# Kernel tuning notes

Measured on AMD Instinct MI355X. Metric: run time of the kernel, lower is better.

Reference implementation:

```python
import jax, jax.numpy as jnp
import numpy as np

EMBED_DIM = 1024
BATCH, SEQ = 4, 2048


def setup_inputs() -> dict:
    key = jax.random.key(0)
    kx, kq, kk, kv = jax.random.split(key, 4)
    return {
        "x": jax.random.normal(kx, (BATCH, SEQ, EMBED_DIM), dtype=jnp.float32),
        "q_weight": jax.random.normal(kq, (EMBED_DIM, EMBED_DIM), dtype=jnp.float32),
        "k_weight": jax.random.normal(kk, (EMBED_DIM, EMBED_DIM), dtype=jnp.float32),
        "v_weight": jax.random.normal(kv, (EMBED_DIM, EMBED_DIM), dtype=jnp.float32),
    }


def reference(x, q_weight, k_weight, v_weight):
    # x: [b, s, d]
    d = x.shape[-1]
    Q = jnp.einsum('bsd,de->bse', x, q_weight)
    K = jnp.einsum('bsd,de->bse', x, k_weight)
    V = jnp.einsum('bsd,de->bse', x, v_weight)
    scores = jnp.einsum('bqe,bke->bqk', Q, K) / jnp.sqrt(jnp.float32(d))
    attn = jax.nn.softmax(scores, axis=-1)
    out = jnp.einsum('bqk,bke->bqe', attn, V)
    return out
```

## Files before the change

### kernel.cpp

```cpp
#include <hip/hip_runtime.h>
#include <hip/hip_bf16.h>


typedef _Float16 half8 __attribute__((ext_vector_type(8)));
typedef _Float16 half4v __attribute__((ext_vector_type(4)));
typedef float f32x16 __attribute__((ext_vector_type(16)));

#define GLOBAL_AS __attribute__((address_space(1)))
#define LDS_AS __attribute__((address_space(3)))

__device__ __forceinline__ void gll16(const _Float16* g, _Float16* l) {
    __builtin_amdgcn_global_load_lds((GLOBAL_AS const void*)g, (LDS_AS void*)l, 16, 0, 0);
}

__device__ __forceinline__ void lgkm0_pin() {
    asm volatile("s_waitcnt lgkmcnt(0)" ::: "memory");
    __builtin_amdgcn_sched_barrier(0);
}

template <int N>
__device__ __forceinline__ void vmwait() {
    if constexpr (N == 0) asm volatile("s_waitcnt vmcnt(0)" ::: "memory");
    else if constexpr (N == 4) asm volatile("s_waitcnt vmcnt(4)" ::: "memory");
    else asm volatile("s_waitcnt vmcnt(8)" ::: "memory");
}

template <int NPROD, int OUTMODE>
__global__ __launch_bounds__(256) void gemm_nt(
    const _Float16* __restrict__ A0, const _Float16* __restrict__ A1,
    const _Float16* __restrict__ B0, const _Float16* __restrict__ B1,
    float* __restrict__ Cf, _Float16* __restrict__ C0, _Float16* __restrict__ C1,
    int lda, int ldb, int ldc, int K,
    long sA, long sB, long sC, float scale, float scale2) {
    constexpr int NTILES = (NPROD == 3) ? 4 : 2;
    constexpr int BUFH = NTILES * 4096;
    __shared__ alignas(16) _Float16 smem[2 * BUFH];

    const int tid = threadIdx.x;
    const int wave = tid >> 6, lane = tid & 63;
    const int wm = (wave >> 1) * 64, wn = (wave & 1) * 64;
    const int q2 = lane >> 5, r32 = lane & 31;

    const long zA = (long)blockIdx.z * sA;
    const long zB = (long)blockIdx.z * sB;
    const long zC = (long)blockIdx.z * sC;

    const float sc = (blockIdx.y * 2 < gridDim.y) ? scale : scale2;

    const int trow = tid >> 2;
    const int tcol = (((tid & 3) - ((tid >> 3) & 3) - ((tid >> 6) & 3)) & 3) * 8;
    const _Float16* gA0 = A0 + zA + (long)(blockIdx.x * 128 + trow) * lda + tcol;
    const _Float16* gB0 = B0 + zB + (long)(blockIdx.y * 128 + trow) * ldb + tcol;
    const _Float16* gA1 = (NPROD == 3) ? (A1 + zA + (long)(blockIdx.x * 128 + trow) * lda + tcol) : nullptr;
    const _Float16* gB1 = (NPROD == 3) ? (B1 + zB + (long)(blockIdx.y * 128 + trow) * ldb + tcol) : nullptr;

    f32x16 acc[2][2];
#pragma unroll
    for (int i = 0; i < 2; ++i)
#pragma unroll
        for (int j = 0; j < 2; ++j)
#pragma unroll
            for (int r = 0; r < 16; ++r) acc[i][j][r] = 0.f;

    const int ldsoff = tid * 8;
    const int fbase = q2 + (r32 >> 1) + (r32 >> 4);

    {
        _Float16* s = smem;
        gll16(gA0, s + ldsoff);
        gll16(gA0 + 64 * lda, s + ldsoff + 2048);
        gll16(gB0, s + 4096 + ldsoff);
        gll16(gB0 + 64 * ldb, s + 4096 + ldsoff + 2048);
        if (NPROD == 3) {
            gll16(gA1, s + 8192 + ldsoff);
            gll16(gA1 + 64 * lda, s + 8192 + ldsoff + 2048);
            gll16(gB1, s + 12288 + ldsoff);
            gll16(gB1 + 64 * ldb, s + 12288 + ldsoff + 2048);
        }
        gA0 += 32; gB0 += 32;
        if (NPROD == 3) { gA1 += 32; gB1 += 32; }
    }

    int buf = 0;
    for (int k0 = 0; k0 < K; k0 += 32) {
        __syncthreads();

        if (k0 + 32 < K) {
            _Float16* s = smem + (buf ^ 1) * BUFH;
            gll16(gA0, s + ldsoff);
            gll16(gA0 + 64 * lda, s + ldsoff + 2048);
            gll16(gB0, s + 4096 + ldsoff);
            gll16(gB0 + 64 * ldb, s + 4096 + ldsoff + 2048);
            if (NPROD == 3) {
                gll16(gA1, s + 8192 + ldsoff);
                gll16(gA1 + 64 * lda, s + 8192 + ldsoff + 2048);
                gll16(gB1, s + 12288 + ldsoff);
                gll16(gB1 + 64 * ldb, s + 12288 + ldsoff + 2048);
            }
            gA0 += 32; gB0 += 32;
            if (NPROD == 3) { gA1 += 32; gB1 += 32; }
        }

        _Float16* sA0 = smem + buf * BUFH;
        _Float16* sB0 = sA0 + 4096;
        _Float16* sA1 = (NPROD == 3) ? sA0 + 8192 : sA0;
        _Float16* sB1 = (NPROD == 3) ? sA0 + 12288 : sA0;
#pragma unroll
        for (int h = 0; h < 2; ++h) {
            half8 a0[2], b0[2], a1[2], b1[2];
#pragma unroll
            for (int i = 0; i < 2; ++i) {
                const int pp = ((fbase + 2 * i + 2 * h) & 3) * 8;
                a0[i] = *(const half8*)(sA0 + (wm + i * 32 + r32) * 32 + pp);
                b0[i] = *(const half8*)(sB0 + (wn + i * 32 + r32) * 32 + pp);
                if (NPROD == 3) {
                    a1[i] = *(const half8*)(sA1 + (wm + i * 32 + r32) * 32 + pp);
                    b1[i] = *(const half8*)(sB1 + (wn + i * 32 + r32) * 32 + pp);
                }
            }
#pragma unroll
            for (int i = 0; i < 2; ++i)
#pragma unroll
                for (int j = 0; j < 2; ++j) {
                    acc[i][j] = __builtin_amdgcn_mfma_f32_32x32x16_f16(a0[i], b0[j], acc[i][j], 0, 0, 0);
                    if (NPROD == 3) {
                        acc[i][j] = __builtin_amdgcn_mfma_f32_32x32x16_f16(a0[i], b1[j], acc[i][j], 0, 0, 0);
                        acc[i][j] = __builtin_amdgcn_mfma_f32_32x32x16_f16(a1[i], b0[j], acc[i][j], 0, 0, 0);
                    }
                }
        }
        buf ^= 1;
    }

    const int crow0 = blockIdx.x * 128 + wm + 4 * q2;
    const int ccol0 = blockIdx.y * 128 + wn + r32;
#pragma unroll
    for (int i = 0; i < 2; ++i)
#pragma unroll
        for (int j = 0; j < 2; ++j)
#pragma unroll
            for (int r = 0; r < 16; ++r) {
                int row = crow0 + i * 32 + (r & 3) + 8 * (r >> 2);
                long off = zC + (long)row * ldc + (ccol0 + j * 32);
                float v = acc[i][j][r] * sc;
                if (OUTMODE == 0) {
                    Cf[off] = v;
                } else if (OUTMODE == 2) {
                    C0[off] = (_Float16)v;
                } else {
                    _Float16 h = (_Float16)v;
                    C0[off] = h;
                    C1[off] = (_Float16)(v - (float)h);
                }
            }
}

__device__ __forceinline__ void ld_a(half8 (&d)[4][2], const _Float16* base,
                                     int wm, int r32, int fbase) {
#pragma unroll
    for (int i = 0; i < 4; ++i)
#pragma unroll
        for (int h = 0; h < 2; ++h)
            d[i][h] = *(const half8*)(base + (wm + 32 * i + r32) * 32 +
                                      ((fbase + 2 * i + 2 * h) & 3) * 8);
}

__device__ __forceinline__ void ld_b(half8 (&d)[2][2], const _Float16* base,
                                     int wn, int r32, int fbase) {
#pragma unroll
    for (int j = 0; j < 2; ++j)
#pragma unroll
        for (int h = 0; h < 2; ++h)
            d[j][h] = *(const half8*)(base + (wn + 32 * j + r32) * 32 +
                                      ((fbase + 2 * j + 2 * h) & 3) * 8);
}

__device__ __forceinline__ void mfma_blk(f32x16 (&acc)[4][2], const half8 (&a)[4][2],
                                         const half8 (&b)[2][2]) {
#pragma unroll
    for (int i = 0; i < 4; ++i)
#pragma unroll
        for (int j = 0; j < 2; ++j) {
            acc[i][j] = __builtin_amdgcn_mfma_f32_32x32x16_f16(a[i][0], b[j][0], acc[i][j], 0, 0, 0);
            acc[i][j] = __builtin_amdgcn_mfma_f32_32x32x16_f16(a[i][1], b[j][1], acc[i][j], 0, 0, 0);
        }
}

__device__ __forceinline__ void stage_tile(_Float16* dst, const _Float16* g, int ld,
                                           int ldsoff) {
    gll16(g, dst + ldsoff);
    gll16(g + (long)128 * ld, dst + 4096 + ldsoff);
}

template <int OUTMODE>
__global__ __launch_bounds__(512, 2) void gemm8p(
    const _Float16* __restrict__ A0, const _Float16* __restrict__ A1,
    const _Float16* __restrict__ B0, const _Float16* __restrict__ B1,
    float* __restrict__ Cf, _Float16* __restrict__ C0, _Float16* __restrict__ C1,
    int lda, int ldb, int ldc, int K,
    long sA, long sB, long sC, float scale, float scale2) {
    __shared__ alignas(16) _Float16 smem[65536];

    const int tid = threadIdx.x;
    const int wave = tid >> 6, lane = tid & 63;
    const int wm = (wave >> 2) * 128, wn = (wave & 3) * 64;
    const int q2 = lane >> 5, r32 = lane & 31;

    const long zA = (long)blockIdx.z * sA;
    const long zB = (long)blockIdx.z * sB;
    const long zC = (long)blockIdx.z * sC;
    const float sc = (blockIdx.y * 2 < gridDim.y) ? scale : scale2;

    const int trow = tid >> 2;
    const int tcol = (((tid & 3) - ((tid >> 3) & 3) - ((tid >> 6) & 3)) & 3) * 8;
    const _Float16* gA0 = A0 + zA + (long)(blockIdx.x * 256 + trow) * lda + tcol;
    const _Float16* gB0 = B0 + zB + (long)(blockIdx.y * 256 + trow) * ldb + tcol;
    const _Float16* gA1 = A1 + zA + (long)(blockIdx.x * 256 + trow) * lda + tcol;
    const _Float16* gB1 = B1 + zB + (long)(blockIdx.y * 256 + trow) * ldb + tcol;

    const int ldsoff = tid * 8;
    const int fbase = q2 + (r32 >> 1) + (r32 >> 4);

    f32x16 acc[4][2];
#pragma unroll
    for (int i = 0; i < 4; ++i)
#pragma unroll
        for (int j = 0; j < 2; ++j)
#pragma unroll
            for (int r = 0; r < 16; ++r) acc[i][j][r] = 0.f;

    const int nT = K >> 5;

    {
        _Float16* s = smem;
        stage_tile(s + 0, gA0, lda, ldsoff);
        stage_tile(s + 8192, gB0, ldb, ldsoff);
        stage_tile(s + 16384, gA1, lda, ldsoff);
        stage_tile(s + 24576, gB1, ldb, ldsoff);
        gA0 += 32; gB0 += 32; gA1 += 32; gB1 += 32;
        vmwait<0>();
        __builtin_amdgcn_s_barrier();
    }

    int buf = 0;
    for (int t = 0; t < nT; ++t) {
        _Float16* scur = smem + buf * 32768;
        _Float16* snx = smem + (buf ^ 1) * 32768;
        const bool pre = (t + 1 < nT);

        half8 a0[4][2], b0[2][2], a1[4][2], b1[2][2];

        ld_a(a0, scur, wm, r32, fbase);
        ld_b(b0, scur + 8192, wn, r32, fbase);
        if (pre) {
            stage_tile(snx + 0, gA0, lda, ldsoff);
            stage_tile(snx + 8192, gB0, ldb, ldsoff);
            stage_tile(snx + 16384, gA1, lda, ldsoff);
            stage_tile(snx + 24576, gB1, ldb, ldsoff);
            gA0 += 32; gB0 += 32; gA1 += 32; gB1 += 32;
        }
        __builtin_amdgcn_s_barrier();
        lgkm0_pin();
        __builtin_amdgcn_s_setprio(1);
        mfma_blk(acc, a0, b0);
        __builtin_amdgcn_s_setprio(0);
        __builtin_amdgcn_s_barrier();

        ld_b(b1, scur + 24576, wn, r32, fbase);
        __builtin_amdgcn_s_barrier();
        lgkm0_pin();
        __builtin_amdgcn_s_setprio(1);
        mfma_blk(acc, a0, b1);
        __builtin_amdgcn_s_setprio(0);
        __builtin_amdgcn_s_barrier();

        ld_a(a1, scur + 16384, wm, r32, fbase);
        __builtin_amdgcn_s_barrier();
        lgkm0_pin();
        __builtin_amdgcn_s_setprio(1);
        mfma_blk(acc, a1, b0);
        __builtin_amdgcn_s_setprio(0);
        if (pre) vmwait<0>();
        __builtin_amdgcn_s_barrier();

        buf ^= 1;
    }

    const int crow0 = blockIdx.x * 256 + wm + 4 * q2;
    const int ccol0 = blockIdx.y * 256 + wn + r32;
#pragma unroll
    for (int i = 0; i < 4; ++i)
#pragma unroll
        for (int j = 0; j < 2; ++j)
#pragma unroll
            for (int r = 0; r < 16; ++r) {
                int row = crow0 + i * 32 + (r & 3) + 8 * (r >> 2);
                long off = zC + (long)row * ldc + (ccol0 + j * 32);
                float v = acc[i][j][r] * sc;
                if (OUTMODE == 0) {
                    Cf[off] = v;
                } else {
                    _Float16 h = (_Float16)v;
                    C0[off] = h;
                    C1[off] = (_Float16)(v - (float)h);
                }
            }
}

__global__ __launch_bounds__(256) void prep_fused(
    const float* __restrict__ x, _Float16* __restrict__ x0, _Float16* __restrict__ x1,
    long n4, int nsplit,
    const float* __restrict__ wq, const float* __restrict__ wk,
    const float* __restrict__ wv,
    _Float16* __restrict__ qk0, _Float16* __restrict__ qk1,
    _Float16* __restrict__ v0, _Float16* __restrict__ v1) {
    __shared__ float t[32][33];
    if ((int)blockIdx.x < nsplit) {
        long i = (long)blockIdx.x * 256 + threadIdx.x;
        if (i >= n4) return;
        float4 v = ((const float4*)x)[i];
        float a[4] = {v.x, v.y, v.z, v.w};
        half4v h, l;
#pragma unroll
        for (int c = 0; c < 4; ++c) {
            h[c] = (_Float16)a[c];
            l[c] = (_Float16)(a[c] - (float)h[c]);
        }
        ((half4v*)x0)[i] = h;
        ((half4v*)x1)[i] = l;
        return;
    }
    const int idx = blockIdx.x - nsplit;
    const int z = idx >> 10;
    const int tile = idx & 1023;
    const float* in = (z == 0) ? wq : (z == 1) ? wk : wv;
    _Float16* o0 = (z == 0) ? qk0 : (z == 1) ? qk0 + 1024 * 1024 : v0;
    _Float16* o1 = (z == 0) ? qk1 : (z == 1) ? qk1 + 1024 * 1024 : v1;

    const int c0 = (tile & 31) * 32, r0 = (tile >> 5) * 32;
    const int tx = threadIdx.x & 31, ty = threadIdx.x >> 5;
#pragma unroll
    for (int i = 0; i < 32; i += 8)
        t[ty + i][tx] = in[(long)(r0 + ty + i) * 1024 + c0 + tx];
    __syncthreads();
#pragma unroll
    for (int i = 0; i < 32; i += 8) {
        float v = t[tx][ty + i];
        _Float16 h = (_Float16)v;
        long o = (long)(c0 + ty + i) * 1024 + r0 + tx;
        o0[o] = h;
        o1[o] = (_Float16)(v - (float)h);
    }
}

__global__ __launch_bounds__(256) void softmax_rows(const float* __restrict__ S,
                                                    _Float16* __restrict__ P) {
    const int n = 2048;
    const long base = (long)blockIdx.x * n;
    const float4* row4 = (const float4*)(S + base);
    const int tid = threadIdx.x;
    const int wave = tid >> 6;

    float4 v0 = row4[tid * 2];
    float4 v1 = row4[tid * 2 + 1];
    float v[8] = {v0.x, v0.y, v0.z, v0.w, v1.x, v1.y, v1.z, v1.w};
    float lm = -3.4e38f;
#pragma unroll
    for (int t = 0; t < 8; ++t) lm = fmaxf(lm, v[t]);
#pragma unroll
    for (int o = 32; o > 0; o >>= 1) lm = fmaxf(lm, __shfl_xor(lm, o));
    __shared__ float redm[4];
    __shared__ float reds[4];
    if ((tid & 63) == 0) redm[wave] = lm;
    __syncthreads();
    lm = fmaxf(fmaxf(redm[0], redm[1]), fmaxf(redm[2], redm[3]));

    float e[8];
    float ls = 0.f;
#pragma unroll
    for (int t = 0; t < 8; ++t) {
        e[t] = __expf(v[t] - lm);
        ls += e[t];
    }
#pragma unroll
    for (int o = 32; o > 0; o >>= 1) ls += __shfl_xor(ls, o);
    if ((tid & 63) == 0) reds[wave] = ls;
    __syncthreads();
    ls = reds[0] + reds[1] + reds[2] + reds[3];
    const float inv = 1.f / ls;
    half8 p;
#pragma unroll
    for (int t = 0; t < 8; ++t) p[t] = (_Float16)(e[t] * inv);
    ((half8*)(P + base))[tid] = p;
}

extern "C" void kernel_launch(void* const* d_in, const int* in_sizes, int n_in,
                              void* d_out, int out_size, void* d_ws, size_t ws_size,
                              hipStream_t stream) {
    (void)in_sizes; (void)n_in; (void)out_size; (void)ws_size;
    const float* x = (const float*)d_in[0];
    const float* wq = (const float*)d_in[1];
    const float* wk = (const float*)d_in[2];
    const float* wv = (const float*)d_in[3];
    float* out = (float*)d_out;
    char* ws = (char*)d_ws;

    const long MB = 1l << 20;
    _Float16* Wqk0 = (_Float16*)(ws + 0 * MB);
    _Float16* Wqk1 = (_Float16*)(ws + 4 * MB);
    _Float16* Wv0  = (_Float16*)(ws + 8 * MB);
    _Float16* Wv1  = (_Float16*)(ws + 10 * MB);
    _Float16* x0   = (_Float16*)(ws + 12 * MB);
    _Float16* x1   = (_Float16*)(ws + 28 * MB);
    _Float16* P    = (_Float16*)(ws + 12 * MB);
    _Float16* QK0  = (_Float16*)(ws + 44 * MB);
    _Float16* QK1  = (_Float16*)(ws + 76 * MB);
    _Float16* Vt   = (_Float16*)(ws + 108 * MB);
    float*    S    = (float*)(ws + 124 * MB);

    const int B = 4, SEQ = 2048, D = 1024;
    const long M = (long)B * SEQ;
    const long ssq = (long)SEQ * SEQ;
    const int nsplit = (int)((M * D / 4 + 255) / 256);

    prep_fused<<<dim3(nsplit + 3072), dim3(256), 0, stream>>>(
        x, x0, x1, M * D / 4, nsplit, wq, wk, wv, Wqk0, Wqk1, Wv0, Wv1);

    gemm8p<1><<<dim3(32, 8, 1), dim3(512), 0, stream>>>(
        x0, x1, Wqk0, Wqk1, nullptr, QK0, QK1, D, D, 2 * D, D,
        0, 0, 0, 0.03125f, 1.0f);

    gemm_nt<1, 2><<<dim3(8, 64, 1), dim3(256), 0, stream>>>(
        Wv0, nullptr, x0, nullptr, nullptr, Vt, nullptr, D, D, (int)M, D,
        0, 0, 0, 1.0f, 1.0f);

    gemm8p<0><<<dim3(8, 8, B), dim3(512), 0, stream>>>(
        QK0, QK1, QK0 + D, QK1 + D, S, nullptr, nullptr, 2 * D, 2 * D, SEQ, D,
        (long)SEQ * 2 * D, (long)SEQ * 2 * D, ssq, 1.0f, 1.0f);

    softmax_rows<<<dim3(B * SEQ), dim3(256), 0, stream>>>(S, P);

    gemm_nt<1, 0><<<dim3(16, 8, B), dim3(256), 0, stream>>>(
        P, nullptr, Vt, nullptr, out, nullptr, nullptr, SEQ, (int)M, D, SEQ,
        ssq, (long)SEQ, (long)SEQ * D, 1.0f, 1.0f);
}
```

Measured before the change: 382.0 us.

## Switch split-fp16 GEMM to 16x16x32 MFMA with five-phase interleaved pipeline

Moves the 3-product split-precision GEMM from 32x32x16 MFMA fragments to 16x16x32 fragments and restructures each K-step into five LDS-load/MFMA phases. The global-to-LDS staging of the next tile is spread across phases instead of being issued all at once. The aim is finer interleaving of LDS reads, global loads and matrix ops so fewer waves stall. It adds barriers per iteration and changes the fragment swizzle and output mapping, which could cost LDS bank conflicts or extra sync overhead.

```diff
diff --git a/kernel.cpp b/kernel.cpp
--- a/kernel.cpp
+++ b/kernel.cpp
@@ -5,6 +5,7 @@
 typedef _Float16 half8 __attribute__((ext_vector_type(8)));
 typedef _Float16 half4v __attribute__((ext_vector_type(4)));
 typedef float f32x16 __attribute__((ext_vector_type(16)));
+typedef float f32x4 __attribute__((ext_vector_type(4)));
 
 #define GLOBAL_AS __attribute__((address_space(1)))
 #define LDS_AS __attribute__((address_space(3)))
@@ -18,11 +19,8 @@
     __builtin_amdgcn_sched_barrier(0);
 }
 
-template <int N>
-__device__ __forceinline__ void vmwait() {
-    if constexpr (N == 0) asm volatile("s_waitcnt vmcnt(0)" ::: "memory");
-    else if constexpr (N == 4) asm volatile("s_waitcnt vmcnt(4)" ::: "memory");
-    else asm volatile("s_waitcnt vmcnt(8)" ::: "memory");
+__device__ __forceinline__ void vmwait0() {
+    asm volatile("s_waitcnt vmcnt(0)" ::: "memory");
 }
 
 template <int NPROD, int OUTMODE>
@@ -155,35 +153,26 @@
             }
 }
 
-__device__ __forceinline__ void ld_a(half8 (&d)[4][2], const _Float16* base,
-                                     int wm, int r32, int fbase) {
+__device__ __forceinline__ int frag_off(int fb, int lrow, int lc) {
+    return (fb + lrow) * 32 + ((((fb >> 4) + lc + (lrow >> 1)) & 3) << 3);
+}
+
+__device__ __forceinline__ void ld4(half8 (&d)[4], const _Float16* base, int fb0,
+                                    int lrow, int lc) {
+#pragma unroll
+    for (int f = 0; f < 4; ++f)
+        d[f] = *(const half8*)(base + frag_off(fb0 + 16 * f, lrow, lc));
+}
+
+template <int MH>
+__device__ __forceinline__ void mm16(f32x4 (&acc)[8][4], const half8 (&a)[4],
+                                     const half8 (&b)[4]) {
 #pragma unroll
     for (int i = 0; i < 4; ++i)
 #pragma unroll
-        for (int h = 0; h < 2; ++h)
-            d[i][h] = *(const half8*)(base + (wm + 32 * i + r32) * 32 +
-                                      ((fbase + 2 * i + 2 * h) & 3) * 8);
-}
-
-__device__ __forceinline__ void ld_b(half8 (&d)[2][2], const _Float16* base,
-                                     int wn, int r32, int fbase) {
-#pragma unroll
-    for (int j = 0; j < 2; ++j)
-#pragma unroll
-        for (int h = 0; h < 2; ++h)
-            d[j][h] = *(const half8*)(base + (wn + 32 * j + r32) * 32 +
-                                      ((fbase + 2 * j + 2 * h) & 3) * 8);
-}
-
-__device__ __forceinline__ void mfma_blk(f32x16 (&acc)[4][2], const half8 (&a)[4][2],
-                                         const half8 (&b)[2][2]) {
-#pragma unroll
-    for (int i = 0; i < 4; ++i)
-#pragma unroll
-        for (int j = 0; j < 2; ++j) {
-            acc[i][j] = __builtin_amdgcn_mfma_f32_32x32x16_f16(a[i][0], b[j][0], acc[i][j], 0, 0, 0);
-            acc[i][j] = __builtin_amdgcn_mfma_f32_32x32x16_f16(a[i][1], b[j][1], acc[i][j], 0, 0, 0);
-        }
+        for (int j = 0; j < 4; ++j)
+            acc[MH * 4 + i][j] =
+                __builtin_amdgcn_mfma_f32_16x16x32_f16(a[i], b[j], acc[MH * 4 + i][j], 0, 0, 0);
 }
 
 __device__ __forceinline__ void stage_tile(_Float16* dst, const _Float16* g, int ld,
@@ -193,7 +182,7 @@
 }
 
 template <int OUTMODE>
-__global__ __launch_bounds__(512, 2) void gemm8p(
+__global__ __launch_bounds__(512, 2) void gemm5p(
     const _Float16* __restrict__ A0, const _Float16* __restrict__ A1,
     const _Float16* __restrict__ B0, const _Float16* __restrict__ B1,
     float* __restrict__ Cf, _Float16* __restrict__ C0, _Float16* __restrict__ C1,
@@ -204,7 +193,7 @@
     const int tid = threadIdx.x;
     const int wave = tid >> 6, lane = tid & 63;
     const int wm = (wave >> 2) * 128, wn = (wave & 3) * 64;
-    const int q2 = lane >> 5, r32 = lane & 31;
+    const int lrow = lane & 15, lc = lane >> 4;
 
     const long zA = (long)blockIdx.z * sA;
     const long zB = (long)blockIdx.z * sB;
@@ -219,15 +208,14 @@
     const _Float16* gB1 = B1 + zB + (long)(blockIdx.y * 256 + trow) * ldb + tcol;
 
     const int ldsoff = tid * 8;
-    const int fbase = q2 + (r32 >> 1) + (r32 >> 4);
-
-    f32x16 acc[4][2];
-#pragma unroll
-    for (int i = 0; i < 4; ++i)
-#pragma unroll
-        for (int j = 0; j < 2; ++j)
-#pragma unroll
-            for (int r = 0; r < 16; ++r) acc[i][j][r] = 0.f;
+
+    f32x4 acc[8][4];
+#pragma unroll
+    for (int i = 0; i < 8; ++i)
+#pragma unroll
+        for (int j = 0; j < 4; ++j)
+#pragma unroll
+            for (int r = 0; r < 4; ++r) acc[i][j][r] = 0.f;
 
     const int nT = K >> 5;
 
@@ -238,7 +226,7 @@
         stage_tile(s + 16384, gA1, lda, ldsoff);
         stage_tile(s + 24576, gB1, ldb, ldsoff);
         gA0 += 32; gB0 += 32; gA1 += 32; gB1 += 32;
-        vmwait<0>();
+        vmwait0();
         __builtin_amdgcn_s_barrier();
     }
 
@@ -248,55 +236,71 @@
         _Float16* snx = smem + (buf ^ 1) * 32768;
         const bool pre = (t + 1 < nT);
 
-        half8 a0[4][2], b0[2][2], a1[4][2], b1[2][2];
-
-        ld_a(a0, scur, wm, r32, fbase);
-        ld_b(b0, scur + 8192, wn, r32, fbase);
-        if (pre) {
-            stage_tile(snx + 0, gA0, lda, ldsoff);
-            stage_tile(snx + 8192, gB0, ldb, ldsoff);
-            stage_tile(snx + 16384, gA1, lda, ldsoff);
-            stage_tile(snx + 24576, gB1, ldb, ldsoff);
-            gA0 += 32; gB0 += 32; gA1 += 32; gB1 += 32;
-        }
+        half8 a0L[4], a0H[4], a1L[4], a1H[4], b0[4], b1[4];
+
+        ld4(a0L, scur, wm, lrow, lc);
+        ld4(b0, scur + 8192, wn, lrow, lc);
+        if (pre) { stage_tile(snx + 0, gA0, lda, ldsoff); gA0 += 32; }
         __builtin_amdgcn_s_barrier();
         lgkm0_pin();
         __builtin_amdgcn_s_setprio(1);
-        mfma_blk(acc, a0, b0);
+        mm16<0>(acc, a0L, b0);
         __builtin_amdgcn_s_setprio(0);
         __builtin_amdgcn_s_barrier();
 
-        ld_b(b1, scur + 24576, wn, r32, fbase);
+        ld4(a0H, scur, wm + 64, lrow, lc);
+        if (pre) { stage_tile(snx + 8192, gB0, ldb, ldsoff); gB0 += 32; }
         __builtin_amdgcn_s_barrier();
         lgkm0_pin();
         __builtin_amdgcn_s_setprio(1);
-        mfma_blk(acc, a0, b1);
+        mm16<1>(acc, a0H, b0);
         __builtin_amdgcn_s_setprio(0);
         __builtin_amdgcn_s_barrier();
 
-        ld_a(a1, scur + 16384, wm, r32, fbase);
+        ld4(b1, scur + 24576, wn, lrow, lc);
+        if (pre) {
+            stage_tile(snx + 16384, gA1, lda, ldsoff); gA1 += 32;
+            stage_tile(snx + 24576, gB1, ldb, ldsoff); gB1 += 32;
+        }
         __builtin_amdgcn_s_barrier();
         lgkm0_pin();
         __builtin_amdgcn_s_setprio(1);
-        mfma_blk(acc, a1, b0);
+        mm16<1>(acc, a0H, b1);
         __builtin_amdgcn_s_setprio(0);
-        if (pre) vmwait<0>();
+        __builtin_amdgcn_s_barrier();
+
+        ld4(a1L, scur + 16384, wm, lrow, lc);
+        __builtin_amdgcn_s_barrier();
+        lgkm0_pin();
+        __builtin_amdgcn_s_setprio(1);
+        mm16<0>(acc, a0L, b1);
+        __builtin_amdgcn_s_setprio(0);
+        __builtin_amdgcn_s_barrier();
+
+        ld4(a1H, scur + 16384, wm + 64, lrow, lc);
+        __builtin_amdgcn_s_barrier();
+        lgkm0_pin();
+        __builtin_amdgcn_s_setprio(1);
+        mm16<0>(acc, a1L, b0);
+        mm16<1>(acc, a1H, b0);
+        __builtin_amdgcn_s_setprio(0);
+        if (pre) vmwait0();
         __builtin_amdgcn_s_barrier();
 
         buf ^= 1;
     }
 
-    const int crow0 = blockIdx.x * 256 + wm + 4 * q2;
-    const int ccol0 = blockIdx.y * 256 + wn + r32;
-#pragma unroll
-    for (int i = 0; i < 4; ++i)
-#pragma unroll
-        for (int j = 0; j < 2; ++j)
-#pragma unroll
-            for (int r = 0; r < 16; ++r) {
-                int row = crow0 + i * 32 + (r & 3) + 8 * (r >> 2);
-                long off = zC + (long)row * ldc + (ccol0 + j * 32);
-                float v = acc[i][j][r] * sc;
+    const int crow0 = blockIdx.x * 256 + wm + lc * 4;
+    const int ccol0 = blockIdx.y * 256 + wn + lrow;
+#pragma unroll
+    for (int mf = 0; mf < 8; ++mf)
+#pragma unroll
+        for (int nf = 0; nf < 4; ++nf)
+#pragma unroll
+            for (int r = 0; r < 4; ++r) {
+                int row = crow0 + mf * 16 + r;
+                long off = zC + (long)row * ldc + (ccol0 + nf * 16);
+                float v = acc[mf][nf][r] * sc;
                 if (OUTMODE == 0) {
                     Cf[off] = v;
                 } else {
@@ -426,7 +430,7 @@
     prep_fused<<<dim3(nsplit + 3072), dim3(256), 0, stream>>>(
         x, x0, x1, M * D / 4, nsplit, wq, wk, wv, Wqk0, Wqk1, Wv0, Wv1);
 
-    gemm8p<1><<<dim3(32, 8, 1), dim3(512), 0, stream>>>(
+    gemm5p<1><<<dim3(32, 8, 1), dim3(512), 0, stream>>>(
         x0, x1, Wqk0, Wqk1, nullptr, QK0, QK1, D, D, 2 * D, D,
         0, 0, 0, 0.03125f, 1.0f);
 
@@ -434,7 +438,7 @@
         Wv0, nullptr, x0, nullptr, nullptr, Vt, nullptr, D, D, (int)M, D,
         0, 0, 0, 1.0f, 1.0f);
 
-    gemm8p<0><<<dim3(8, 8, B), dim3(512), 0, stream>>>(
+    gemm5p<0><<<dim3(8, 8, B), dim3(512), 0, stream>>>(
         QK0, QK1, QK0 + D, QK1 + D, S, nullptr, nullptr, 2 * D, 2 * D, SEQ, D,
         (long)SEQ * 2 * D, (long)SEQ * 2 * D, ssq, 1.0f, 1.0f);
 
```

After: 362.8 us. 1.05x faster.

## Restructure split-product GEMM pipeline with staggered prefetch and fewer barriers

Applied to the files above, without the earlier changes.

The main loop of the three-product fp16 GEMM used six barriers per K-step, each paired with an lgkmcnt wait. It now uses two. The next tile's loads are split into two halves, issued before the first and second MFMA phases. Partial vmcnt(4) waits let the A0/B0 half land while the A1/B1 half is still in flight, and the second and third MFMA blocks are merged into one phase. The goal is to cut synchronization stalls and overlap global-to-LDS traffic with compute, at the cost of tighter reliance on exact in-flight load counts.

```diff
diff --git a/kernel.cpp b/kernel.cpp
--- a/kernel.cpp
+++ b/kernel.cpp
@@ -5,6 +5,7 @@
 typedef _Float16 half8 __attribute__((ext_vector_type(8)));
 typedef _Float16 half4v __attribute__((ext_vector_type(4)));
 typedef float f32x16 __attribute__((ext_vector_type(16)));
+typedef float f32x4 __attribute__((ext_vector_type(4)));
 
 #define GLOBAL_AS __attribute__((address_space(1)))
 #define LDS_AS __attribute__((address_space(3)))
@@ -18,11 +19,16 @@
     __builtin_amdgcn_sched_barrier(0);
 }
 
-template <int N>
-__device__ __forceinline__ void vmwait() {
-    if constexpr (N == 0) asm volatile("s_waitcnt vmcnt(0)" ::: "memory");
-    else if constexpr (N == 4) asm volatile("s_waitcnt vmcnt(4)" ::: "memory");
-    else asm volatile("s_waitcnt vmcnt(8)" ::: "memory");
+__device__ __forceinline__ void barrier_fence() {
+    asm volatile("s_barrier" ::: "memory");
+}
+
+__device__ __forceinline__ void vmwait0() {
+    asm volatile("s_waitcnt vmcnt(0)" ::: "memory");
+}
+
+__device__ __forceinline__ void vmwait4() {
+    asm volatile("s_waitcnt vmcnt(4)" ::: "memory");
 }
 
 template <int NPROD, int OUTMODE>
@@ -175,8 +181,8 @@
                                       ((fbase + 2 * j + 2 * h) & 3) * 8);
 }
 
-__device__ __forceinline__ void mfma_blk(f32x16 (&acc)[4][2], const half8 (&a)[4][2],
-                                         const half8 (&b)[2][2]) {
+__device__ __forceinline__ void mm32(f32x16 (&acc)[4][2], const half8 (&a)[4][2],
+                                     const half8 (&b)[2][2]) {
 #pragma unroll
     for (int i = 0; i < 4; ++i)
 #pragma unroll
@@ -193,7 +199,7 @@
 }
 
 template <int OUTMODE>
-__global__ __launch_bounds__(512, 2) void gemm8p(
+__global__ __launch_bounds__(512, 2) void gemm5p(
     const _Float16* __restrict__ A0, const _Float16* __restrict__ A1,
     const _Float16* __restrict__ B0, const _Float16* __restrict__ B1,
     float* __restrict__ Cf, _Float16* __restrict__ C0, _Float16* __restrict__ C1,
@@ -238,8 +244,8 @@
         stage_tile(s + 16384, gA1, lda, ldsoff);
         stage_tile(s + 24576, gB1, ldb, ldsoff);
         gA0 += 32; gB0 += 32; gA1 += 32; gB1 += 32;
-        vmwait<0>();
-        __builtin_amdgcn_s_barrier();
+        vmwait4();
+        barrier_fence();
     }
 
     int buf = 0;
@@ -248,40 +254,36 @@
         _Float16* snx = smem + (buf ^ 1) * 32768;
         const bool pre = (t + 1 < nT);
 
-        half8 a0[4][2], b0[2][2], a1[4][2], b1[2][2];
+        half8 a0[4][2], a1[4][2], b0[2][2], b1[2][2];
 
         ld_a(a0, scur, wm, r32, fbase);
         ld_b(b0, scur + 8192, wn, r32, fbase);
         if (pre) {
-            stage_tile(snx + 0, gA0, lda, ldsoff);
-            stage_tile(snx + 8192, gB0, ldb, ldsoff);
-            stage_tile(snx + 16384, gA1, lda, ldsoff);
-            stage_tile(snx + 24576, gB1, ldb, ldsoff);
-            gA0 += 32; gB0 += 32; gA1 += 32; gB1 += 32;
-        }
-        __builtin_amdgcn_s_barrier();
-        lgkm0_pin();
+            stage_tile(snx + 0, gA0, lda, ldsoff); gA0 += 32;
+            stage_tile(snx + 8192, gB0, ldb, ldsoff); gB0 += 32;
+        }
         __builtin_amdgcn_s_setprio(1);
-        mfma_blk(acc, a0, b0);
+        mm32(acc, a0, b0);
         __builtin_amdgcn_s_setprio(0);
-        __builtin_amdgcn_s_barrier();
+        if (pre) vmwait4();
+        else vmwait0();
+        barrier_fence();
 
         ld_b(b1, scur + 24576, wn, r32, fbase);
-        __builtin_amdgcn_s_barrier();
-        lgkm0_pin();
+        ld_a(a1, scur + 16384, wm, r32, fbase);
+        if (pre) {
+            stage_tile(snx + 16384, gA1, lda, ldsoff); gA1 += 32;
+            stage_tile(snx + 24576, gB1, ldb, ldsoff); gB1 += 32;
+        }
         __builtin_amdgcn_s_setprio(1);
-        mfma_blk(acc, a0, b1);
+        mm32(acc, a0, b1);
+        mm32(acc, a1, b0);
         __builtin_amdgcn_s_setprio(0);
-        __builtin_amdgcn_s_barrier();
-
-        ld_a(a1, scur + 16384, wm, r32, fbase);
-        __builtin_amdgcn_s_barrier();
-        lgkm0_pin();
-        __builtin_amdgcn_s_setprio(1);
-        mfma_blk(acc, a1, b0);
-        __builtin_amdgcn_s_setprio(0);
-        if (pre) vmwait<0>();
-        __builtin_amdgcn_s_barrier();
+        if (pre) {
+            lgkm0_pin();
+            vmwait4();
+            barrier_fence();
+        }
 
         buf ^= 1;
     }
@@ -426,7 +428,7 @@
     prep_fused<<<dim3(nsplit + 3072), dim3(256), 0, stream>>>(
         x, x0, x1, M * D / 4, nsplit, wq, wk, wv, Wqk0, Wqk1, Wv0, Wv1);
 
-    gemm8p<1><<<dim3(32, 8, 1), dim3(512), 0, stream>>>(
+    gemm5p<1><<<dim3(32, 8, 1), dim3(512), 0, stream>>>(
         x0, x1, Wqk0, Wqk1, nullptr, QK0, QK1, D, D, 2 * D, D,
         0, 0, 0, 0.03125f, 1.0f);
 
@@ -434,7 +436,7 @@
         Wv0, nullptr, x0, nullptr, nullptr, Vt, nullptr, D, D, (int)M, D,
         0, 0, 0, 1.0f, 1.0f);
 
-    gemm8p<0><<<dim3(8, 8, B), dim3(512), 0, stream>>>(
+    gemm5p<0><<<dim3(8, 8, B), dim3(512), 0, stream>>>(
         QK0, QK1, QK0 + D, QK1 + D, S, nullptr, nullptr, 2 * D, 2 * D, SEQ, D,
         (long)SEQ * 2 * D, (long)SEQ * 2 * D, ssq, 1.0f, 1.0f);
 
```

Measured after the change: 378.3 us. No clear change (-1.0%).
